# Performance work log

Hardware: AMD Instinct MI355X
Metric: run time of the kernel (lower is better)

## Reference

```python
import jax, jax.numpy as jnp
import numpy as np

B, L, HID, LOW = 1024, 64, 512, 20
TEMP = 1.0
EPS = 1e-20


def setup_inputs() -> dict:
    key = jax.random.key(0)
    ks = jax.random.split(key, 8)
    input_h = jax.random.normal(ks[0], (B, L, HID), jnp.float32)
    input_c = jax.random.normal(ks[1], (B, L, HID), jnp.float32)
    length = jax.random.randint(ks[2], (B,), L // 2, L + 1)          # valid lengths in [L/2, L]
    u_noise = jax.random.uniform(ks[3], (L - 1, B, L - 1), jnp.float32)  # gumbel uniforms per level
    s = 1.0 / np.sqrt(HID)
    W_reduce = jax.random.uniform(ks[4], (HID, LOW), jnp.float32, -s, s)
    b_reduce = jnp.zeros((LOW,), jnp.float32)
    s2 = 1.0 / np.sqrt(2 * LOW)
    W_comp = jax.random.uniform(ks[5], (2 * LOW, 5 * LOW), jnp.float32, -s2, s2)
    b_comp = jnp.zeros((5 * LOW,), jnp.float32)
    query = jax.random.normal(ks[6], (LOW,), jnp.float32) / np.sqrt(LOW)
    return dict(input_h=input_h, input_c=input_c, W_reduce=W_reduce, b_reduce=b_reduce,
                W_comp=W_comp, b_comp=b_comp, query=query, u_noise=u_noise, length=length)


def _treelstm(hl, cl, hr, cr, W, b):
    # BinaryTreeLSTMLayer.forward: concat children, one Linear to 5 gates
    v = jnp.concatenate([hl, hr], axis=-1) @ W + b          # (B, n, 5*LOW)
    i_, fl, fr, u_, o = jnp.split(v, 5, axis=-1)
    c = cl * jax.nn.sigmoid(fl + 1.0) + cr * jax.nn.sigmoid(fr + 1.0) \
        + jnp.tanh(u_) * jax.nn.sigmoid(i_)
    h = jax.nn.sigmoid(o) * jnp.tanh(c)
    return h, c


def _masked_softmax(logits, mask):
    probs = jax.nn.softmax(logits, axis=1)
    probs = probs * mask + EPS
    return probs / probs.sum(axis=1, keepdims=True)


def _st_gumbel(logits, u, mask):
    g = -jnp.log(-jnp.log(u + EPS) + EPS)                   # gumbel noise (non-diff, matches .data)
    y = _masked_softmax((logits + g) / TEMP, mask)
    y_hard = jax.nn.one_hot(jnp.argmax(y, axis=1), y.shape[1], dtype=y.dtype)
    return jax.lax.stop_gradient(y_hard - y) + y            # straight-through


def _forward(input_h, input_c, W_reduce, b_reduce, W_comp, b_comp, query, u_noise, length):
    h = input_h @ W_reduce + b_reduce                       # (B, L, LOW)  reduce_dim
    c = input_c @ W_reduce + b_reduce
    length_mask = (jnp.arange(L)[None, :] < length[:, None]).astype(h.dtype)  # (B, L)
    for i in range(L - 1):                                  # sequential DP over pyramid levels
        hl, cl = h[:, :-1], c[:, :-1]
        hr, cr = h[:, 1:], c[:, 1:]
        nh, nc = _treelstm(hl, cl, hr, cr, W_comp, b_comp)  # (B, L-1-i, LOW) all adjacent merges
        if i < L - 2:
            logits = nh @ query                             # dot_nd scoring, (B, L-1-i)
            sel = _st_gumbel(logits, u_noise[i, :, :L - 1 - i], length_mask[:, i + 1:])
            cum = jnp.cumsum(sel, axis=1)
            left = (1.0 - cum)[..., None]                   # keep old left spans
            right = (cum - sel)[..., None]                  # shift old right spans
            se = sel[..., None]
            nh = se * nh + left * hl + right * hr
            nc = se * nc + left * cl + right * cr
        done = length_mask[:, i + 1][:, None, None]         # update_state done_mask
        h = done * nh + (1.0 - done) * hl
        c = done * nc + (1.0 - done) * cl
    return h[:, 0]                                          # (B, LOW) root hidden state


def reference(input_h, input_c, W_reduce, b_reduce, W_comp, b_comp, query, u_noise, length):
    return _forward(input_h, input_c, W_reduce, b_reduce, W_comp, b_comp, query, u_noise, length)
```

## Files before the change

kernel.cpp:

```cpp
#include <hip/hip_runtime.h>
#include <cmath>
#include <cfloat>

namespace {

constexpr int kB   = 1024;
constexpr int kL   = 64;
constexpr int kHid = 512;
constexpr int kLow = 20;
constexpr int kLM1 = 63;
constexpr int kRowElems = kL * kLow;

typedef float v2f __attribute__((ext_vector_type(2)));

__device__ __forceinline__ float fsig(float x) {
  return __builtin_amdgcn_rcpf(1.0f + __expf(-x));
}
__device__ __forceinline__ float ftanhf(float x) {
  return 1.0f - 2.0f * __builtin_amdgcn_rcpf(1.0f + __expf(2.0f * x));
}
__device__ __forceinline__ int rdl_i(int v, int l) {
  return __builtin_amdgcn_readlane(v, l);
}
__device__ __forceinline__ float rdl_f(float v, int l) {
  return __int_as_float(__builtin_amdgcn_readlane(__float_as_int(v), l));
}

#define DPPI(v, ctrl) __builtin_amdgcn_update_dpp((v), (v), (ctrl), 0xF, 0xF, false)
#define DPPF(v, ctrl) __int_as_float(DPPI(__float_as_int(v), (ctrl)))
#define DPPF0(v, ctrl)                                                        \
  __int_as_float(__builtin_amdgcn_update_dpp(0, __float_as_int(v), (ctrl),    \
                                             0xF, 0xF, true))
#define UMAX_STAGE(CTRL)                                                      \
  {                                                                           \
    const unsigned o_ = (unsigned)DPPI((int)m, CTRL);                         \
    m = (m > o_) ? m : o_;                                                    \
  }

#define PKFMA(ACC, X, W)                                                      \
  asm("v_pk_fma_f32 %0, %1, %2, %0" : "+v"(ACC) : "v"(X), "v"(W))

#define LOGIT_REDUCE(PR_)                                                     \
  {                                                                           \
    PR_ += DPPF0(PR_, 0xB1);                                                  \
    PR_ += DPPF0(PR_, 0x4E);                                                  \
    PR_ += DPPF0(PR_, 0x141);                                                 \
    PR_ += DPPF0(PR_, 0x140);                                                 \
    PR_ += DPPF0(PR_, 0x142);                                                 \
  }

__global__ __launch_bounds__(256, 6)
void reduce_kernel(const float* __restrict__ Xh, const float* __restrict__ Xc,
                   const float* __restrict__ W, const float* __restrict__ bv,
                   float* __restrict__ H0, float* __restrict__ C0) {
  __shared__ float xs[5184];
  __shared__ float wsm[64 * 20];

  const int bid = blockIdx.x;
  const float* __restrict__ X = (bid < kB) ? Xh : Xc;
  float* __restrict__ O       = (bid < kB) ? H0 : C0;
  const int b = bid & (kB - 1);
  X += (size_t)b * kL * kHid;
  O += (size_t)b * kRowElems;

  const int tid  = threadIdx.x;
  const int wave = tid >> 6;
  const int lane = tid & 63;

  float acc[20];
#pragma unroll
  for (int d = 0; d < 20; ++d) acc[d] = 0.0f;

  for (int ch = 0; ch < 8; ++ch) {
    __syncthreads();
#pragma unroll
    for (int r = 0; r < 4; ++r) {
      int f   = r * 256 + tid;
      int row = f >> 4;
      int c4  = (f & 15) << 2;
      float4 v = *(const float4*)(X + row * kHid + ch * 64 + c4);
      *(float4*)(xs + row * 65 + c4) = v;
    }
#pragma unroll
    for (int r = 0; r < 5; ++r) {
      int f = r * 256 + tid;
      wsm[f] = W[ch * 1280 + f];
    }
    __syncthreads();
#pragma unroll
    for (int kk = 0; kk < 16; ++kk) {
      int k = wave * 16 + kk;
      float x = xs[lane * 65 + k];
      const float4* wp = (const float4*)(wsm + k * 20);
      float4 w0 = wp[0], w1 = wp[1], w2 = wp[2], w3 = wp[3], w4 = wp[4];
      acc[0]  = fmaf(x, w0.x, acc[0]);  acc[1]  = fmaf(x, w0.y, acc[1]);
      acc[2]  = fmaf(x, w0.z, acc[2]);  acc[3]  = fmaf(x, w0.w, acc[3]);
      acc[4]  = fmaf(x, w1.x, acc[4]);  acc[5]  = fmaf(x, w1.y, acc[5]);
      acc[6]  = fmaf(x, w1.z, acc[6]);  acc[7]  = fmaf(x, w1.w, acc[7]);
      acc[8]  = fmaf(x, w2.x, acc[8]);  acc[9]  = fmaf(x, w2.y, acc[9]);
      acc[10] = fmaf(x, w2.z, acc[10]); acc[11] = fmaf(x, w2.w, acc[11]);
      acc[12] = fmaf(x, w3.x, acc[12]); acc[13] = fmaf(x, w3.y, acc[13]);
      acc[14] = fmaf(x, w3.z, acc[14]); acc[15] = fmaf(x, w3.w, acc[15]);
      acc[16] = fmaf(x, w4.x, acc[16]); acc[17] = fmaf(x, w4.y, acc[17]);
      acc[18] = fmaf(x, w4.z, acc[18]); acc[19] = fmaf(x, w4.w, acc[19]);
    }
  }

  __syncthreads();
  float* red = xs;
#pragma unroll
  for (int d = 0; d < 20; ++d) red[wave * 1280 + lane * 20 + d] = acc[d];
  __syncthreads();
#pragma unroll
  for (int r = 0; r < 5; ++r) {
    int f = r * 256 + tid;
    float s = (red[f] + red[1280 + f]) + (red[2560 + f] + red[3840 + f]);
    O[f] = s + bv[f % 20];
  }
}

#define EVAL_UNIT(A_, B2_, PS_, DD_, HN_)                                     \
  {                                                                           \
    float ai = bcs[DD_], af = bcs[20 + DD_], ag = bcs[40 + DD_],              \
          au = bcs[60 + DD_], ao = bcs[80 + DD_];                             \
    const int xa_ = (A_)*20, xb_ = (B2_)*20, wr_ = (DD_)*44;                  \
    _Pragma("unroll")                                                         \
    for (int kq = 0; kq < 10; ++kq) {                                         \
      const float4 xq = (kq < 5)                                              \
          ? *(const float4*)(h_state + xa_ + kq * 4)                          \
          : *(const float4*)(h_state + xb_ + (kq - 5) * 4);                   \
      const float4 wi = *(const float4*)(Wt + wr_ + kq * 4);                  \
      const float4 wf = *(const float4*)(Wt + 880  + wr_ + kq * 4);           \
      const float4 wg = *(const float4*)(Wt + 1760 + wr_ + kq * 4);           \
      const float4 wu = *(const float4*)(Wt + 2640 + wr_ + kq * 4);           \
      const float4 wo = *(const float4*)(Wt + 3520 + wr_ + kq * 4);           \
      ai = fmaf(xq.x, wi.x, ai); ai = fmaf(xq.y, wi.y, ai);                   \
      ai = fmaf(xq.z, wi.z, ai); ai = fmaf(xq.w, wi.w, ai);                   \
      af = fmaf(xq.x, wf.x, af); af = fmaf(xq.y, wf.y, af);                   \
      af = fmaf(xq.z, wf.z, af); af = fmaf(xq.w, wf.w, af);                   \
      ag = fmaf(xq.x, wg.x, ag); ag = fmaf(xq.y, wg.y, ag);                   \
      ag = fmaf(xq.z, wg.z, ag); ag = fmaf(xq.w, wg.w, ag);                   \
      au = fmaf(xq.x, wu.x, au); au = fmaf(xq.y, wu.y, au);                   \
      au = fmaf(xq.z, wu.z, au); au = fmaf(xq.w, wu.w, au);                   \
      ao = fmaf(xq.x, wo.x, ao); ao = fmaf(xq.y, wo.y, ao);                   \
      ao = fmaf(xq.z, wo.z, ao); ao = fmaf(xq.w, wo.w, ao);                   \
    }                                                                         \
    const float cl_ = c_state[(A_)*20 + (DD_)],                               \
                cr_ = c_state[(B2_)*20 + (DD_)];                              \
    const float cn_ = cl_ * fsig(af + 1.0f) + cr_ * fsig(ag + 1.0f) +         \
                      ftanhf(au) * fsig(ai);                                  \
    (HN_) = fsig(ao) * ftanhf(cn_);                                           \
    nh[(PS_)*20 + (DD_)] = (HN_);                                             \
    nc[(PS_)*20 + (DD_)] = cn_;                                               \
  }

__global__ __launch_bounds__(64, 1)
void pyramid_kernel(const float* __restrict__ H0, const float* __restrict__ C0,
                    const float* __restrict__ Wc, const float* __restrict__ bcg,
                    const float* __restrict__ query, const float* __restrict__ U,
                    const int* __restrict__ length, float* __restrict__ out) {
  __shared__ float h_state[64 * 20];
  __shared__ float c_state[64 * 20];
  __shared__ float nh[63 * 20];
  __shared__ float nc[63 * 20];
  __shared__ float Wt[100 * 44];
  __shared__ float bcs[100];
  __shared__ float qvs[20];
  __shared__ float sc[200];

  const int b    = blockIdx.x;
  const int lane = threadIdx.x;
  const int p    = lane >> 5;
  const int dd   = lane & 31;
  const int ddc  = dd < 20 ? dd : 19;
  int len = length[b];
  len = len < 1 ? 1 : (len > 64 ? 64 : len);

  {
    const float4* h4 = (const float4*)(H0 + (size_t)b * kRowElems);
    const float4* c4 = (const float4*)(C0 + (size_t)b * kRowElems);
#pragma unroll
    for (int r = 0; r < 5; ++r) {
      int f = r * 64 + lane;
      ((float4*)h_state)[f] = h4[f];
      ((float4*)c_state)[f] = c4[f];
    }
  }
  for (int f = lane; f < 4000; f += 64) {
    int c = f / 40, k = f - c * 40;
    Wt[c * 44 + k] = Wc[k * 100 + c];
  }
  for (int f = lane; f < 100; f += 64) bcs[f] = bcg[f];
  if (lane < 20) qvs[lane] = query[lane];

  const bool cact = lane < 50;
  const int  c0   = cact ? 2 * lane : 0;
  const int  c1   = c0 + 1;
  v2f Wv0[20], Wv1[20];
#pragma unroll
  for (int k2 = 0; k2 < 20; ++k2) {
    Wv0[k2] = (v2f){Wc[(2 * k2) * 100 + c0], Wc[(2 * k2 + 1) * 100 + c0]};
    Wv1[k2] = (v2f){Wc[(2 * k2) * 100 + c1], Wc[(2 * k2 + 1) * 100 + c1]};
  }
  const float bb0 = bcg[c0], bb1 = bcg[c1];
  const float qv_r = query[ddc];

  int   idx_r  = lane;
  int   pidx_r = lane;
  float lgt_r  = -FLT_MAX;

  const int col = lane < 62 ? lane : 62;
  const float u_row0 = U[b * kLM1 + col];
  float u_c = (kLM1 > 1) ? U[1 * (kB * kLM1) + b * kLM1 + col] : 0.0f;

#pragma unroll 1
  for (int r = 0; r < 20; ++r) {
    int uu = r * 64 + lane;
    if (uu < 1260) {
      int pp = uu / 20, d2 = uu - pp * 20;
      float hn_;
      EVAL_UNIT(pp, pp + 1, pp, d2, hn_);
      (void)hn_;
    }
  }
  if (lane < 63) {
    float s = 0.0f;
#pragma unroll
    for (int q = 0; q < 5; ++q) {
      const float4 t  = *(const float4*)(nh  + lane * 20 + q * 4);
      const float4 qv = *(const float4*)(qvs + q * 4);
      s = fmaf(t.x, qv.x, s); s = fmaf(t.y, qv.y, s);
      s = fmaf(t.z, qv.z, s); s = fmaf(t.w, qv.w, s);
    }
    lgt_r = s;
  }

  float gcur = -__logf(-__logf(u_row0 + 1e-20f) + 1e-20f);

  const int nIter = len - 1;
#pragma unroll 1
  for (int i = 0; i < nIter; ++i) {
    const int n = kL - i;

    const float zf = lgt_r + gcur;
    const unsigned ub = __float_as_uint(zf);
    unsigned key = ((int)ub < 0) ? ~ub : (ub | 0x80000000u);
    const bool valid = (lane <= n - 2) && ((i + 1 + lane) < len);
    if (!valid) key = 0u;
    unsigned m = key;
    UMAX_STAGE(0xB1);
    UMAX_STAGE(0x4E);
    UMAX_STAGE(0x141);
    UMAX_STAGE(0x140);
    UMAX_STAGE(0x142);
    UMAX_STAGE(0x143);
    const unsigned gmax = (unsigned)rdl_i((int)m, 63);
    const unsigned long long bal = __ballot(valid && (key == gmax));
    const int k = (int)(__ffsll(bal) - 1);

    float u_d = 0.0f;
    if (i + 2 <= kLM1 - 1) u_d = U[(i + 2) * (kB * kLM1) + b * kLM1 + col];

    const int km1 = (k >= 1) ? k - 1 : 0;
    const int kp2 = (k <= n - 3) ? k + 2 : 0;
    const int tgt = rdl_i(idx_r,  k);
    const int psk = rdl_i(pidx_r, k);
    const int iA  = rdl_i(idx_r,  km1);
    const int pA  = rdl_i(pidx_r, km1);
    const int iB  = rdl_i(idx_r,  kp2);

    if (lane < 20) {
      h_state[tgt * 20 + lane] = nh[psk * 20 + lane];
      c_state[tgt * 20 + lane] = nc[psk * 20 + lane];
    }

    {
      int   sI = DPPI(idx_r,  0x101);
      int   sP = DPPI(pidx_r, 0x101);
      float sL = DPPF(lgt_r,  0x101);
      const int   bi16 = rdl_i(idx_r, 16),  bi32 = rdl_i(idx_r, 32),
                  bi48 = rdl_i(idx_r, 48);
      const int   bp16 = rdl_i(pidx_r, 16), bp32 = rdl_i(pidx_r, 32),
                  bp48 = rdl_i(pidx_r, 48);
      const float bl16 = rdl_f(lgt_r, 16),  bl32 = rdl_f(lgt_r, 32),
                  bl48 = rdl_f(lgt_r, 48);
      if (lane == 15) { sI = bi16; sP = bp16; sL = bl16; }
      if (lane == 31) { sI = bi32; sP = bp32; sL = bl32; }
      if (lane == 47) { sI = bi48; sP = bp48; sL = bl48; }
      const bool doI = (lane >= k + 1) && (lane <= n - 2);
      const bool doP = (lane >= k + 1) && (lane <= n - 3);
      if (doI) idx_r = sI;
      if (doP) { pidx_r = sP; lgt_r = sL; }
    }

    if (i < len - 2) {
      const bool hasA = (k >= 1);
      const bool hasB = (k <= n - 3);

      v2f hA2[10], hT2[10], hB2[10];
#pragma unroll
      for (int q = 0; q < 5; ++q) {
        const float4 tA = *(const float4*)(h_state + iA * 20 + q * 4);
        const float4 tT = *(const float4*)(nh + psk * 20 + q * 4);
        const float4 tB = *(const float4*)(h_state + iB * 20 + q * 4);
        hA2[2*q]   = (v2f){tA.x, tA.y};  hA2[2*q+1] = (v2f){tA.z, tA.w};
        hT2[2*q]   = (v2f){tT.x, tT.y};  hT2[2*q+1] = (v2f){tT.z, tT.w};
        hB2[2*q]   = (v2f){tB.x, tB.y};  hB2[2*q+1] = (v2f){tB.z, tB.w};
      }

      v2f aA0 = (v2f){0.f, 0.f}, aA1 = aA0, aB0 = aA0, aB1 = aA0;
#pragma unroll
      for (int k2 = 0; k2 < 10; ++k2) {
        PKFMA(aA0, hA2[k2], Wv0[k2]);
        PKFMA(aA1, hA2[k2], Wv1[k2]);
        PKFMA(aB0, hT2[k2], Wv0[k2]);
        PKFMA(aB1, hT2[k2], Wv1[k2]);
      }
#pragma unroll
      for (int k2 = 10; k2 < 20; ++k2) {
        PKFMA(aA0, hT2[k2 - 10], Wv0[k2]);
        PKFMA(aA1, hT2[k2 - 10], Wv1[k2]);
        PKFMA(aB0, hB2[k2 - 10], Wv0[k2]);
        PKFMA(aB1, hB2[k2 - 10], Wv1[k2]);
      }

      if (cact) {
        *(v2f*)(sc + c0)       = (v2f){aA0[0] + aA0[1] + bb0,
                                       aA1[0] + aA1[1] + bb1};
        *(v2f*)(sc + 100 + c0) = (v2f){aB0[0] + aB0[1] + bb0,
                                       aB1[0] + aB1[1] + bb1};
      }

      const float* scp = sc + p * 100;
      const float i_ = scp[ddc],      fl_ = scp[20 + ddc],
                  fr_ = scp[40 + ddc], u_ = scp[60 + ddc],
                  o_ = scp[80 + ddc];
      const float cl_ = (p == 0) ? c_state[iA * 20 + ddc] : nc[psk * 20 + ddc];
      const float cr_ = (p == 0) ? nc[psk * 20 + ddc] : c_state[iB * 20 + ddc];
      const float cn_ = cl_ * fsig(fl_ + 1.0f) + cr_ * fsig(fr_ + 1.0f) +
                        ftanhf(u_) * fsig(i_);
      const float hn_ = fsig(o_) * ftanhf(cn_);
      const int   slot = (p == 0) ? pA : psk;
      const bool  mine = (p == 0) ? hasA : hasB;
      if (mine && dd < 20) {
        nh[slot * 20 + dd] = hn_;
        nc[slot * 20 + dd] = cn_;
      }
      float pr = (dd < 20) ? hn_ * qv_r : 0.0f;
      LOGIT_REDUCE(pr);
      const float vA = rdl_f(pr, 31);
      const float vB = rdl_f(pr, 63);
      if (hasA && lane == k - 1) lgt_r = vA;
      if (hasB && lane == k)     lgt_r = vB;
    }

    gcur = -__logf(-__logf(u_c + 1e-20f) + 1e-20f);
    u_c  = u_d;
  }

  const int root = rdl_i(idx_r, 0);
  if (lane < 20) {
    out[b * 20 + lane] = h_state[root * 20 + lane];
  }
}

}

extern "C" void kernel_launch(void* const* d_in, const int* in_sizes, int n_in,
                              void* d_out, int out_size, void* d_ws, size_t ws_size,
                              hipStream_t stream) {
  const float* input_h  = (const float*)d_in[0];
  const float* input_c  = (const float*)d_in[1];
  const float* W_reduce = (const float*)d_in[2];
  const float* b_reduce = (const float*)d_in[3];
  const float* W_comp   = (const float*)d_in[4];
  const float* b_comp   = (const float*)d_in[5];
  const float* query    = (const float*)d_in[6];
  const float* u_noise  = (const float*)d_in[7];
  const int*   length   = (const int*)d_in[8];
  float* out = (float*)d_out;

  float* H0 = (float*)d_ws;
  float* C0 = H0 + (size_t)kB * kL * kLow;

  reduce_kernel<<<dim3(2 * kB), dim3(256), 0, stream>>>(
      input_h, input_c, W_reduce, b_reduce, H0, C0);
  pyramid_kernel<<<dim3(kB), dim3(64), 0, stream>>>(
      H0, C0, W_comp, b_comp, query, u_noise, length, out);
}
```

Baseline: 159.1 us.

## Read reduce weights via scalar loads and hoist child state loads above writes

In the reduce kernel, the weight tile is no longer staged in shared memory. Each wave now reads its weight row directly from global memory at a wave-uniform address, which lets the compiler use scalar loads, and the inner k loop is kept rolled. In the tree kernel, the loads of the left, target and right child h/c vectors are moved before the state writeback so their LDS latency overlaps the selection bookkeeping. The risk is that the uniform global loads add latency or that the extra live registers lower occupancy. Hoisting the loads above the writes also relies on them reading values that the writeback does not change.

```diff
diff --git a/kernel.cpp b/kernel.cpp
--- a/kernel.cpp
+++ b/kernel.cpp
@@ -54,7 +54,6 @@
                    const float* __restrict__ W, const float* __restrict__ bv,
                    float* __restrict__ H0, float* __restrict__ C0) {
   __shared__ float xs[5184];
-  __shared__ float wsm[64 * 20];
 
   const int bid = blockIdx.x;
   const float* __restrict__ X = (bid < kB) ? Xh : Xc;
@@ -64,7 +63,7 @@
   O += (size_t)b * kRowElems;
 
   const int tid  = threadIdx.x;
-  const int wave = tid >> 6;
+  const int wave = __builtin_amdgcn_readfirstlane(tid >> 6);
   const int lane = tid & 63;
 
   float acc[20];
@@ -81,28 +80,14 @@
       float4 v = *(const float4*)(X + row * kHid + ch * 64 + c4);
       *(float4*)(xs + row * 65 + c4) = v;
     }
-#pragma unroll
-    for (int r = 0; r < 5; ++r) {
-      int f = r * 256 + tid;
-      wsm[f] = W[ch * 1280 + f];
-    }
     __syncthreads();
-#pragma unroll
+#pragma unroll 1
     for (int kk = 0; kk < 16; ++kk) {
-      int k = wave * 16 + kk;
-      float x = xs[lane * 65 + k];
-      const float4* wp = (const float4*)(wsm + k * 20);
-      float4 w0 = wp[0], w1 = wp[1], w2 = wp[2], w3 = wp[3], w4 = wp[4];
-      acc[0]  = fmaf(x, w0.x, acc[0]);  acc[1]  = fmaf(x, w0.y, acc[1]);
-      acc[2]  = fmaf(x, w0.z, acc[2]);  acc[3]  = fmaf(x, w0.w, acc[3]);
-      acc[4]  = fmaf(x, w1.x, acc[4]);  acc[5]  = fmaf(x, w1.y, acc[5]);
-      acc[6]  = fmaf(x, w1.z, acc[6]);  acc[7]  = fmaf(x, w1.w, acc[7]);
-      acc[8]  = fmaf(x, w2.x, acc[8]);  acc[9]  = fmaf(x, w2.y, acc[9]);
-      acc[10] = fmaf(x, w2.z, acc[10]); acc[11] = fmaf(x, w2.w, acc[11]);
-      acc[12] = fmaf(x, w3.x, acc[12]); acc[13] = fmaf(x, w3.y, acc[13]);
-      acc[14] = fmaf(x, w3.z, acc[14]); acc[15] = fmaf(x, w3.w, acc[15]);
-      acc[16] = fmaf(x, w4.x, acc[16]); acc[17] = fmaf(x, w4.y, acc[17]);
-      acc[18] = fmaf(x, w4.z, acc[18]); acc[19] = fmaf(x, w4.w, acc[19]);
+      const int k = wave * 16 + kk;
+      const float x = xs[lane * 65 + k];
+      const float* __restrict__ wr = W + ch * 1280 + k * 20;
+#pragma unroll
+      for (int d = 0; d < 20; ++d) acc[d] = fmaf(x, wr[d], acc[d]);
     }
   }
 
@@ -269,6 +254,20 @@
     const int pA  = rdl_i(pidx_r, km1);
     const int iB  = rdl_i(idx_r,  kp2);
 
+    v2f hA2[10], hT2[10], hB2[10];
+#pragma unroll
+    for (int q = 0; q < 5; ++q) {
+      const float4 tA = *(const float4*)(h_state + iA * 20 + q * 4);
+      const float4 tT = *(const float4*)(nh + psk * 20 + q * 4);
+      const float4 tB = *(const float4*)(h_state + iB * 20 + q * 4);
+      hA2[2*q]   = (v2f){tA.x, tA.y};  hA2[2*q+1] = (v2f){tA.z, tA.w};
+      hT2[2*q]   = (v2f){tT.x, tT.y};  hT2[2*q+1] = (v2f){tT.z, tT.w};
+      hB2[2*q]   = (v2f){tB.x, tB.y};  hB2[2*q+1] = (v2f){tB.z, tB.w};
+    }
+    const float cA_ = c_state[iA * 20 + ddc];
+    const float cT_ = nc[psk * 20 + ddc];
+    const float cB_ = c_state[iB * 20 + ddc];
+
     if (lane < 20) {
       h_state[tgt * 20 + lane] = nh[psk * 20 + lane];
       c_state[tgt * 20 + lane] = nc[psk * 20 + lane];
@@ -297,17 +296,6 @@
       const bool hasA = (k >= 1);
       const bool hasB = (k <= n - 3);
 
-      v2f hA2[10], hT2[10], hB2[10];
-#pragma unroll
-      for (int q = 0; q < 5; ++q) {
-        const float4 tA = *(const float4*)(h_state + iA * 20 + q * 4);
-        const float4 tT = *(const float4*)(nh + psk * 20 + q * 4);
-        const float4 tB = *(const float4*)(h_state + iB * 20 + q * 4);
-        hA2[2*q]   = (v2f){tA.x, tA.y};  hA2[2*q+1] = (v2f){tA.z, tA.w};
-        hT2[2*q]   = (v2f){tT.x, tT.y};  hT2[2*q+1] = (v2f){tT.z, tT.w};
-        hB2[2*q]   = (v2f){tB.x, tB.y};  hB2[2*q+1] = (v2f){tB.z, tB.w};
-      }
-
       v2f aA0 = (v2f){0.f, 0.f}, aA1 = aA0, aB0 = aA0, aB1 = aA0;
 #pragma unroll
       for (int k2 = 0; k2 < 10; ++k2) {
@@ -335,8 +323,8 @@
       const float i_ = scp[ddc],      fl_ = scp[20 + ddc],
                   fr_ = scp[40 + ddc], u_ = scp[60 + ddc],
                   o_ = scp[80 + ddc];
-      const float cl_ = (p == 0) ? c_state[iA * 20 + ddc] : nc[psk * 20 + ddc];
-      const float cr_ = (p == 0) ? nc[psk * 20 + ddc] : c_state[iB * 20 + ddc];
+      const float cl_ = (p == 0) ? cA_ : cT_;
+      const float cr_ = (p == 0) ? cT_ : cB_;
       const float cn_ = cl_ * fsig(fl_ + 1.0f) + cr_ * fsig(fr_ + 1.0f) +
                         ftanhf(u_) * fsig(i_);
       const float hn_ = fsig(o_) * ftanhf(cn_);
```

After: 188.2 us. 1.18x slower.

## Process two batch rows per wavefront to interleave independent serial chains

Applied to the files above, without the earlier changes.

Each 64-lane block now handles two batch rows, A and B, and interleaves their serial pyramid iterations (argmax, merge, shift, packed FMA, nonlinearity) so the latency of one row's dependent steps can be hidden by the other row's instructions. The grid is halved to 512 blocks. In exchange, LDS use per block roughly doubles, register pressure rises, and a pair of rows runs for the longer of their two lengths, with the shorter row masked by active flags. The intent is to raise instruction-level parallelism in this latency-bound sequential loop.

```diff
diff --git a/kernel.cpp b/kernel.cpp
--- a/kernel.cpp
+++ b/kernel.cpp
@@ -119,39 +119,162 @@
   }
 }
 
-#define EVAL_UNIT(A_, B2_, PS_, DD_, HN_)                                     \
-  {                                                                           \
-    float ai = bcs[DD_], af = bcs[20 + DD_], ag = bcs[40 + DD_],              \
-          au = bcs[60 + DD_], ao = bcs[80 + DD_];                             \
-    const int xa_ = (A_)*20, xb_ = (B2_)*20, wr_ = (DD_)*44;                  \
+#define EVAL_UNIT2(PP_, DD_)                                                  \
+  {                                                                           \
+    float aiA = bcs[DD_], afA = bcs[20 + DD_], agA = bcs[40 + DD_],           \
+          auA = bcs[60 + DD_], aoA = bcs[80 + DD_];                           \
+    float aiB = aiA, afB = afA, agB = agA, auB = auA, aoB = aoA;              \
+    const int xa_ = (PP_)*20, xb_ = (PP_ + 1)*20, wr_ = (DD_)*44;             \
     _Pragma("unroll")                                                         \
     for (int kq = 0; kq < 10; ++kq) {                                         \
-      const float4 xq = (kq < 5)                                              \
-          ? *(const float4*)(h_state + xa_ + kq * 4)                          \
-          : *(const float4*)(h_state + xb_ + (kq - 5) * 4);                   \
+      const float4 xqA = (kq < 5)                                             \
+          ? *(const float4*)(h_sA + xa_ + kq * 4)                             \
+          : *(const float4*)(h_sA + xb_ + (kq - 5) * 4);                      \
+      const float4 xqB = (kq < 5)                                             \
+          ? *(const float4*)(h_sB + xa_ + kq * 4)                             \
+          : *(const float4*)(h_sB + xb_ + (kq - 5) * 4);                      \
       const float4 wi = *(const float4*)(Wt + wr_ + kq * 4);                  \
       const float4 wf = *(const float4*)(Wt + 880  + wr_ + kq * 4);           \
       const float4 wg = *(const float4*)(Wt + 1760 + wr_ + kq * 4);           \
       const float4 wu = *(const float4*)(Wt + 2640 + wr_ + kq * 4);           \
       const float4 wo = *(const float4*)(Wt + 3520 + wr_ + kq * 4);           \
-      ai = fmaf(xq.x, wi.x, ai); ai = fmaf(xq.y, wi.y, ai);                   \
-      ai = fmaf(xq.z, wi.z, ai); ai = fmaf(xq.w, wi.w, ai);                   \
-      af = fmaf(xq.x, wf.x, af); af = fmaf(xq.y, wf.y, af);                   \
-      af = fmaf(xq.z, wf.z, af); af = fmaf(xq.w, wf.w, af);                   \
-      ag = fmaf(xq.x, wg.x, ag); ag = fmaf(xq.y, wg.y, ag);                   \
-      ag = fmaf(xq.z, wg.z, ag); ag = fmaf(xq.w, wg.w, ag);                   \
-      au = fmaf(xq.x, wu.x, au); au = fmaf(xq.y, wu.y, au);                   \
-      au = fmaf(xq.z, wu.z, au); au = fmaf(xq.w, wu.w, au);                   \
-      ao = fmaf(xq.x, wo.x, ao); ao = fmaf(xq.y, wo.y, ao);                   \
-      ao = fmaf(xq.z, wo.z, ao); ao = fmaf(xq.w, wo.w, ao);                   \
-    }                                                                         \
-    const float cl_ = c_state[(A_)*20 + (DD_)],                               \
-                cr_ = c_state[(B2_)*20 + (DD_)];                              \
-    const float cn_ = cl_ * fsig(af + 1.0f) + cr_ * fsig(ag + 1.0f) +         \
-                      ftanhf(au) * fsig(ai);                                  \
-    (HN_) = fsig(ao) * ftanhf(cn_);                                           \
-    nh[(PS_)*20 + (DD_)] = (HN_);                                             \
-    nc[(PS_)*20 + (DD_)] = cn_;                                               \
+      aiA = fmaf(xqA.x, wi.x, aiA); aiA = fmaf(xqA.y, wi.y, aiA);             \
+      aiA = fmaf(xqA.z, wi.z, aiA); aiA = fmaf(xqA.w, wi.w, aiA);             \
+      afA = fmaf(xqA.x, wf.x, afA); afA = fmaf(xqA.y, wf.y, afA);             \
+      afA = fmaf(xqA.z, wf.z, afA); afA = fmaf(xqA.w, wf.w, afA);             \
+      agA = fmaf(xqA.x, wg.x, agA); agA = fmaf(xqA.y, wg.y, agA);             \
+      agA = fmaf(xqA.z, wg.z, agA); agA = fmaf(xqA.w, wg.w, agA);             \
+      auA = fmaf(xqA.x, wu.x, auA); auA = fmaf(xqA.y, wu.y, auA);             \
+      auA = fmaf(xqA.z, wu.z, auA); auA = fmaf(xqA.w, wu.w, auA);             \
+      aoA = fmaf(xqA.x, wo.x, aoA); aoA = fmaf(xqA.y, wo.y, aoA);             \
+      aoA = fmaf(xqA.z, wo.z, aoA); aoA = fmaf(xqA.w, wo.w, aoA);             \
+      aiB = fmaf(xqB.x, wi.x, aiB); aiB = fmaf(xqB.y, wi.y, aiB);             \
+      aiB = fmaf(xqB.z, wi.z, aiB); aiB = fmaf(xqB.w, wi.w, aiB);             \
+      afB = fmaf(xqB.x, wf.x, afB); afB = fmaf(xqB.y, wf.y, afB);             \
+      afB = fmaf(xqB.z, wf.z, afB); afB = fmaf(xqB.w, wf.w, afB);             \
+      agB = fmaf(xqB.x, wg.x, agB); agB = fmaf(xqB.y, wg.y, agB);             \
+      agB = fmaf(xqB.z, wg.z, agB); agB = fmaf(xqB.w, wg.w, agB);             \
+      auB = fmaf(xqB.x, wu.x, auB); auB = fmaf(xqB.y, wu.y, auB);             \
+      auB = fmaf(xqB.z, wu.z, auB); auB = fmaf(xqB.w, wu.w, auB);             \
+      aoB = fmaf(xqB.x, wo.x, aoB); aoB = fmaf(xqB.y, wo.y, aoB);             \
+      aoB = fmaf(xqB.z, wo.z, aoB); aoB = fmaf(xqB.w, wo.w, aoB);             \
+    }                                                                         \
+    {                                                                         \
+      const float clA = c_sA[(PP_)*20 + (DD_)],                               \
+                  crA = c_sA[(PP_+1)*20 + (DD_)];                             \
+      const float cnA = clA * fsig(afA + 1.0f) + crA * fsig(agA + 1.0f) +     \
+                        ftanhf(auA) * fsig(aiA);                              \
+      const float hnA = fsig(aoA) * ftanhf(cnA);                              \
+      nhA[(PP_)*20 + (DD_)] = hnA;  ncA[(PP_)*20 + (DD_)] = cnA;              \
+      const float clB = c_sB[(PP_)*20 + (DD_)],                               \
+                  crB = c_sB[(PP_+1)*20 + (DD_)];                             \
+      const float cnB = clB * fsig(afB + 1.0f) + crB * fsig(agB + 1.0f) +     \
+                        ftanhf(auB) * fsig(aiB);                              \
+      const float hnB = fsig(aoB) * ftanhf(cnB);                              \
+      nhB[(PP_)*20 + (DD_)] = hnB;  ncB[(PP_)*20 + (DD_)] = cnB;              \
+    }                                                                         \
+  }
+
+#define ROW_ARGMAX(LGT_, G_, LEN_, KOUT_)                                     \
+  {                                                                           \
+    const float zf = (LGT_) + (G_);                                           \
+    const unsigned ub = __float_as_uint(zf);                                  \
+    unsigned key = ((int)ub < 0) ? ~ub : (ub | 0x80000000u);                  \
+    const bool valid = (lane <= n - 2) && ((i + 1 + lane) < (LEN_));          \
+    if (!valid) key = 0u;                                                     \
+    unsigned m = key;                                                         \
+    UMAX_STAGE(0xB1); UMAX_STAGE(0x4E); UMAX_STAGE(0x141);                    \
+    UMAX_STAGE(0x140); UMAX_STAGE(0x142); UMAX_STAGE(0x143);                  \
+    const unsigned gmax = (unsigned)rdl_i((int)m, 63);                        \
+    const unsigned long long bal = __ballot(valid && (key == gmax));          \
+    (KOUT_) = bal ? (int)(__ffsll(bal) - 1) : 0;                              \
+  }
+
+#define ROW_HOIST(HS, CS, NH, NC, IL_, IR_, PSK_, XL, XT, XR, CL_, CT_, CR_)  \
+  {                                                                           \
+    _Pragma("unroll")                                                         \
+    for (int q = 0; q < 5; ++q) {                                             \
+      const float4 tL = *(const float4*)((HS) + (IL_)*20 + q * 4);            \
+      const float4 tT = *(const float4*)((NH) + (PSK_)*20 + q * 4);           \
+      const float4 tR = *(const float4*)((HS) + (IR_)*20 + q * 4);            \
+      XL[2*q] = (v2f){tL.x, tL.y}; XL[2*q+1] = (v2f){tL.z, tL.w};             \
+      XT[2*q] = (v2f){tT.x, tT.y}; XT[2*q+1] = (v2f){tT.z, tT.w};             \
+      XR[2*q] = (v2f){tR.x, tR.y}; XR[2*q+1] = (v2f){tR.z, tR.w};             \
+    }                                                                         \
+    CL_ = (CS)[(IL_)*20 + ddc];                                               \
+    CT_ = (NC)[(PSK_)*20 + ddc];                                              \
+    CR_ = (CS)[(IR_)*20 + ddc];                                               \
+  }
+
+#define ROW_MERGE(HS, CS, NH, NC, TGT_, PSK_, ACT_)                           \
+  if ((ACT_) && lane < 20) {                                                  \
+    (HS)[(TGT_)*20 + lane] = (NH)[(PSK_)*20 + lane];                          \
+    (CS)[(TGT_)*20 + lane] = (NC)[(PSK_)*20 + lane];                          \
+  }
+
+#define ROW_SHIFT(IDX_, PIDX_, LGT_, K_, ACT_)                                \
+  {                                                                           \
+    int   sI = DPPI(IDX_,  0x101);                                            \
+    int   sP = DPPI(PIDX_, 0x101);                                            \
+    float sL = DPPF(LGT_,  0x101);                                            \
+    const int   b16i = rdl_i(IDX_, 16),  b32i = rdl_i(IDX_, 32),              \
+                b48i = rdl_i(IDX_, 48);                                       \
+    const int   b16p = rdl_i(PIDX_, 16), b32p = rdl_i(PIDX_, 32),             \
+                b48p = rdl_i(PIDX_, 48);                                      \
+    const float b16l = rdl_f(LGT_, 16),  b32l = rdl_f(LGT_, 32),              \
+                b48l = rdl_f(LGT_, 48);                                       \
+    if (lane == 15) { sI = b16i; sP = b16p; sL = b16l; }                      \
+    if (lane == 31) { sI = b32i; sP = b32p; sL = b32l; }                      \
+    if (lane == 47) { sI = b48i; sP = b48p; sL = b48l; }                      \
+    const bool doI = (ACT_) && (lane >= (K_) + 1) && (lane <= n - 2);         \
+    const bool doP = (ACT_) && (lane >= (K_) + 1) && (lane <= n - 3);         \
+    if (doI) IDX_ = sI;                                                       \
+    if (doP) { PIDX_ = sP; LGT_ = sL; }                                       \
+  }
+
+#define ROW_FMASC(XL, XT, XR, SC)                                             \
+  {                                                                           \
+    v2f a0 = (v2f){0.f, 0.f}, a1 = a0, b0 = a0, b1 = a0;                      \
+    _Pragma("unroll")                                                         \
+    for (int k2 = 0; k2 < 10; ++k2) {                                         \
+      PKFMA(a0, XL[k2], Wv0[k2]);                                             \
+      PKFMA(a1, XL[k2], Wv1[k2]);                                             \
+      PKFMA(b0, XT[k2], Wv0[k2]);                                             \
+      PKFMA(b1, XT[k2], Wv1[k2]);                                             \
+    }                                                                         \
+    _Pragma("unroll")                                                         \
+    for (int k2 = 10; k2 < 20; ++k2) {                                        \
+      PKFMA(a0, XT[k2 - 10], Wv0[k2]);                                        \
+      PKFMA(a1, XT[k2 - 10], Wv1[k2]);                                        \
+      PKFMA(b0, XR[k2 - 10], Wv0[k2]);                                        \
+      PKFMA(b1, XR[k2 - 10], Wv1[k2]);                                        \
+    }                                                                         \
+    if (cact) {                                                               \
+      *(v2f*)((SC) + c0)       = (v2f){a0[0]+a0[1]+bb0, a1[0]+a1[1]+bb1};     \
+      *(v2f*)((SC) + 100 + c0) = (v2f){b0[0]+b0[1]+bb0, b1[0]+b1[1]+bb1};     \
+    }                                                                         \
+  }
+
+#define ROW_NONLIN(SC, CL_, CT_, CR_, NH, NC, PL_, PSK_, K_, EV_, LGT_)       \
+  {                                                                           \
+    const bool hasL = (K_) >= 1, hasR = (K_) <= n - 3;                        \
+    const float* scp = (SC) + p * 100;                                        \
+    const float gi = scp[ddc], gfl = scp[20 + ddc], gfr = scp[40 + ddc],      \
+                gu = scp[60 + ddc], go = scp[80 + ddc];                       \
+    const float cl_ = (p == 0) ? (CL_) : (CT_);                               \
+    const float cr_ = (p == 0) ? (CT_) : (CR_);                               \
+    const float cn_ = cl_ * fsig(gfl + 1.0f) + cr_ * fsig(gfr + 1.0f) +       \
+                      ftanhf(gu) * fsig(gi);                                  \
+    const float hn_ = fsig(go) * ftanhf(cn_);                                 \
+    const int   slot = (p == 0) ? (PL_) : (PSK_);                             \
+    const bool  mine = (EV_) && ((p == 0) ? hasL : hasR);                     \
+    if (mine && dd < 20) { (NH)[slot*20 + dd] = hn_; (NC)[slot*20 + dd] = cn_; } \
+    float pr = (dd < 20) ? hn_ * qv_r : 0.0f;                                 \
+    LOGIT_REDUCE(pr);                                                         \
+    const float vL = rdl_f(pr, 31);                                           \
+    const float vR = rdl_f(pr, 63);                                           \
+    if ((EV_) && hasL && lane == (K_) - 1) (LGT_) = vL;                       \
+    if ((EV_) && hasR && lane == (K_))     (LGT_) = vR;                       \
   }
 
 __global__ __launch_bounds__(64, 1)
@@ -159,31 +282,36 @@
                     const float* __restrict__ Wc, const float* __restrict__ bcg,
                     const float* __restrict__ query, const float* __restrict__ U,
                     const int* __restrict__ length, float* __restrict__ out) {
-  __shared__ float h_state[64 * 20];
-  __shared__ float c_state[64 * 20];
-  __shared__ float nh[63 * 20];
-  __shared__ float nc[63 * 20];
+  __shared__ float h_sA[64 * 20], c_sA[64 * 20], nhA[63 * 20], ncA[63 * 20];
+  __shared__ float h_sB[64 * 20], c_sB[64 * 20], nhB[63 * 20], ncB[63 * 20];
   __shared__ float Wt[100 * 44];
   __shared__ float bcs[100];
   __shared__ float qvs[20];
-  __shared__ float sc[200];
-
-  const int b    = blockIdx.x;
+  __shared__ float scA[200], scB[200];
+
+  const int bblk = blockIdx.x;
+  const int rowA = 2 * bblk, rowB = 2 * bblk + 1;
   const int lane = threadIdx.x;
   const int p    = lane >> 5;
   const int dd   = lane & 31;
   const int ddc  = dd < 20 ? dd : 19;
-  int len = length[b];
-  len = len < 1 ? 1 : (len > 64 ? 64 : len);
+  int lenA = length[rowA];
+  lenA = lenA < 1 ? 1 : (lenA > 64 ? 64 : lenA);
+  int lenB = length[rowB];
+  lenB = lenB < 1 ? 1 : (lenB > 64 ? 64 : lenB);
 
   {
-    const float4* h4 = (const float4*)(H0 + (size_t)b * kRowElems);
-    const float4* c4 = (const float4*)(C0 + (size_t)b * kRowElems);
+    const float4* h4A = (const float4*)(H0 + (size_t)rowA * kRowElems);
+    const float4* c4A = (const float4*)(C0 + (size_t)rowA * kRowElems);
+    const float4* h4B = (const float4*)(H0 + (size_t)rowB * kRowElems);
+    const float4* c4B = (const float4*)(C0 + (size_t)rowB * kRowElems);
 #pragma unroll
     for (int r = 0; r < 5; ++r) {
       int f = r * 64 + lane;
-      ((float4*)h_state)[f] = h4[f];
-      ((float4*)c_state)[f] = c4[f];
+      ((float4*)h_sA)[f] = h4A[f];
+      ((float4*)c_sA)[f] = c4A[f];
+      ((float4*)h_sB)[f] = h4B[f];
+      ((float4*)c_sB)[f] = c4B[f];
     }
   }
   for (int f = lane; f < 4000; f += 64) {
@@ -205,162 +333,103 @@
   const float bb0 = bcg[c0], bb1 = bcg[c1];
   const float qv_r = query[ddc];
 
-  int   idx_r  = lane;
-  int   pidx_r = lane;
-  float lgt_r  = -FLT_MAX;
+  int   idxA = lane, pidxA = lane;
+  int   idxB = lane, pidxB = lane;
+  float lgtA = -FLT_MAX, lgtB = -FLT_MAX;
 
   const int col = lane < 62 ? lane : 62;
-  const float u_row0 = U[b * kLM1 + col];
-  float u_c = (kLM1 > 1) ? U[1 * (kB * kLM1) + b * kLM1 + col] : 0.0f;
+  const float u0A = U[rowA * kLM1 + col];
+  const float u0B = U[rowB * kLM1 + col];
+  float u_cA = U[(size_t)1 * (kB * kLM1) + rowA * kLM1 + col];
+  float u_cB = U[(size_t)1 * (kB * kLM1) + rowB * kLM1 + col];
 
 #pragma unroll 1
   for (int r = 0; r < 20; ++r) {
     int uu = r * 64 + lane;
     if (uu < 1260) {
       int pp = uu / 20, d2 = uu - pp * 20;
-      float hn_;
-      EVAL_UNIT(pp, pp + 1, pp, d2, hn_);
-      (void)hn_;
+      EVAL_UNIT2(pp, d2);
     }
   }
   if (lane < 63) {
-    float s = 0.0f;
+    float sA = 0.0f, sB = 0.0f;
 #pragma unroll
     for (int q = 0; q < 5; ++q) {
-      const float4 t  = *(const float4*)(nh  + lane * 20 + q * 4);
       const float4 qv = *(const float4*)(qvs + q * 4);
-      s = fmaf(t.x, qv.x, s); s = fmaf(t.y, qv.y, s);
-      s = fmaf(t.z, qv.z, s); s = fmaf(t.w, qv.w, s);
-    }
-    lgt_r = s;
-  }
-
-  float gcur = -__logf(-__logf(u_row0 + 1e-20f) + 1e-20f);
-
-  const int nIter = len - 1;
+      const float4 tA = *(const float4*)(nhA + lane * 20 + q * 4);
+      const float4 tB = *(const float4*)(nhB + lane * 20 + q * 4);
+      sA = fmaf(tA.x, qv.x, sA); sA = fmaf(tA.y, qv.y, sA);
+      sA = fmaf(tA.z, qv.z, sA); sA = fmaf(tA.w, qv.w, sA);
+      sB = fmaf(tB.x, qv.x, sB); sB = fmaf(tB.y, qv.y, sB);
+      sB = fmaf(tB.z, qv.z, sB); sB = fmaf(tB.w, qv.w, sB);
+    }
+    lgtA = sA;
+    lgtB = sB;
+  }
+
+  float gA = -__logf(-__logf(u0A + 1e-20f) + 1e-20f);
+  float gB = -__logf(-__logf(u0B + 1e-20f) + 1e-20f);
+
+  const int maxIter = (lenA > lenB ? lenA : lenB) - 1;
 #pragma unroll 1
-  for (int i = 0; i < nIter; ++i) {
+  for (int i = 0; i < maxIter; ++i) {
     const int n = kL - i;
-
-    const float zf = lgt_r + gcur;
-    const unsigned ub = __float_as_uint(zf);
-    unsigned key = ((int)ub < 0) ? ~ub : (ub | 0x80000000u);
-    const bool valid = (lane <= n - 2) && ((i + 1 + lane) < len);
-    if (!valid) key = 0u;
-    unsigned m = key;
-    UMAX_STAGE(0xB1);
-    UMAX_STAGE(0x4E);
-    UMAX_STAGE(0x141);
-    UMAX_STAGE(0x140);
-    UMAX_STAGE(0x142);
-    UMAX_STAGE(0x143);
-    const unsigned gmax = (unsigned)rdl_i((int)m, 63);
-    const unsigned long long bal = __ballot(valid && (key == gmax));
-    const int k = (int)(__ffsll(bal) - 1);
-
-    float u_d = 0.0f;
-    if (i + 2 <= kLM1 - 1) u_d = U[(i + 2) * (kB * kLM1) + b * kLM1 + col];
-
-    const int km1 = (k >= 1) ? k - 1 : 0;
-    const int kp2 = (k <= n - 3) ? k + 2 : 0;
-    const int tgt = rdl_i(idx_r,  k);
-    const int psk = rdl_i(pidx_r, k);
-    const int iA  = rdl_i(idx_r,  km1);
-    const int pA  = rdl_i(pidx_r, km1);
-    const int iB  = rdl_i(idx_r,  kp2);
-
-    if (lane < 20) {
-      h_state[tgt * 20 + lane] = nh[psk * 20 + lane];
-      c_state[tgt * 20 + lane] = nc[psk * 20 + lane];
-    }
+    const bool actA = i < lenA - 1, actB = i < lenB - 1;
+    const bool evA  = i < lenA - 2, evB  = i < lenB - 2;
+
+    int kA, kB2;
+    ROW_ARGMAX(lgtA, gA, lenA, kA);
+    ROW_ARGMAX(lgtB, gB, lenB, kB2);
+
+    float u_dA = 0.0f, u_dB = 0.0f;
+    if (i + 2 < kLM1) {
+      u_dA = U[(size_t)(i + 2) * (kB * kLM1) + rowA * kLM1 + col];
+      u_dB = U[(size_t)(i + 2) * (kB * kLM1) + rowB * kLM1 + col];
+    }
+
+    const int A_km1 = kA >= 1 ? kA - 1 : 0;
+    const int A_kp2 = kA <= n - 3 ? kA + 2 : 0;
+    const int A_tgt = rdl_i(idxA, kA),   A_psk = rdl_i(pidxA, kA);
+    const int A_iL  = rdl_i(idxA, A_km1), A_pL = rdl_i(pidxA, A_km1);
+    const int A_iR  = rdl_i(idxA, A_kp2);
+    const int B_km1 = kB2 >= 1 ? kB2 - 1 : 0;
+    const int B_kp2 = kB2 <= n - 3 ? kB2 + 2 : 0;
+    const int B_tgt = rdl_i(idxB, kB2),   B_psk = rdl_i(pidxB, kB2);
+    const int B_iL  = rdl_i(idxB, B_km1), B_pL = rdl_i(pidxB, B_km1);
+    const int B_iR  = rdl_i(idxB, B_kp2);
 
     {
-      int   sI = DPPI(idx_r,  0x101);
-      int   sP = DPPI(pidx_r, 0x101);
-      float sL = DPPF(lgt_r,  0x101);
-      const int   bi16 = rdl_i(idx_r, 16),  bi32 = rdl_i(idx_r, 32),
-                  bi48 = rdl_i(idx_r, 48);
-      const int   bp16 = rdl_i(pidx_r, 16), bp32 = rdl_i(pidx_r, 32),
-                  bp48 = rdl_i(pidx_r, 48);
-      const float bl16 = rdl_f(lgt_r, 16),  bl32 = rdl_f(lgt_r, 32),
-                  bl48 = rdl_f(lgt_r, 48);
-      if (lane == 15) { sI = bi16; sP = bp16; sL = bl16; }
-      if (lane == 31) { sI = bi32; sP = bp32; sL = bl32; }
-      if (lane == 47) { sI = bi48; sP = bp48; sL = bl48; }
-      const bool doI = (lane >= k + 1) && (lane <= n - 2);
-      const bool doP = (lane >= k + 1) && (lane <= n - 3);
-      if (doI) idx_r = sI;
-      if (doP) { pidx_r = sP; lgt_r = sL; }
-    }
-
-    if (i < len - 2) {
-      const bool hasA = (k >= 1);
-      const bool hasB = (k <= n - 3);
-
-      v2f hA2[10], hT2[10], hB2[10];
-#pragma unroll
-      for (int q = 0; q < 5; ++q) {
-        const float4 tA = *(const float4*)(h_state + iA * 20 + q * 4);
-        const float4 tT = *(const float4*)(nh + psk * 20 + q * 4);
-        const float4 tB = *(const float4*)(h_state + iB * 20 + q * 4);
-        hA2[2*q]   = (v2f){tA.x, tA.y};  hA2[2*q+1] = (v2f){tA.z, tA.w};
-        hT2[2*q]   = (v2f){tT.x, tT.y};  hT2[2*q+1] = (v2f){tT.z, tT.w};
-        hB2[2*q]   = (v2f){tB.x, tB.y};  hB2[2*q+1] = (v2f){tB.z, tB.w};
-      }
-
-      v2f aA0 = (v2f){0.f, 0.f}, aA1 = aA0, aB0 = aA0, aB1 = aA0;
-#pragma unroll
-      for (int k2 = 0; k2 < 10; ++k2) {
-        PKFMA(aA0, hA2[k2], Wv0[k2]);
-        PKFMA(aA1, hA2[k2], Wv1[k2]);
-        PKFMA(aB0, hT2[k2], Wv0[k2]);
-        PKFMA(aB1, hT2[k2], Wv1[k2]);
-      }
-#pragma unroll
-      for (int k2 = 10; k2 < 20; ++k2) {
-        PKFMA(aA0, hT2[k2 - 10], Wv0[k2]);
-        PKFMA(aA1, hT2[k2 - 10], Wv1[k2]);
-        PKFMA(aB0, hB2[k2 - 10], Wv0[k2]);
-        PKFMA(aB1, hB2[k2 - 10], Wv1[k2]);
-      }
-
-      if (cact) {
-        *(v2f*)(sc + c0)       = (v2f){aA0[0] + aA0[1] + bb0,
-                                       aA1[0] + aA1[1] + bb1};
-        *(v2f*)(sc + 100 + c0) = (v2f){aB0[0] + aB0[1] + bb0,
-                                       aB1[0] + aB1[1] + bb1};
-      }
-
-      const float* scp = sc + p * 100;
-      const float i_ = scp[ddc],      fl_ = scp[20 + ddc],
-                  fr_ = scp[40 + ddc], u_ = scp[60 + ddc],
-                  o_ = scp[80 + ddc];
-      const float cl_ = (p == 0) ? c_state[iA * 20 + ddc] : nc[psk * 20 + ddc];
-      const float cr_ = (p == 0) ? nc[psk * 20 + ddc] : c_state[iB * 20 + ddc];
-      const float cn_ = cl_ * fsig(fl_ + 1.0f) + cr_ * fsig(fr_ + 1.0f) +
-                        ftanhf(u_) * fsig(i_);
-      const float hn_ = fsig(o_) * ftanhf(cn_);
-      const int   slot = (p == 0) ? pA : psk;
-      const bool  mine = (p == 0) ? hasA : hasB;
-      if (mine && dd < 20) {
-        nh[slot * 20 + dd] = hn_;
-        nc[slot * 20 + dd] = cn_;
-      }
-      float pr = (dd < 20) ? hn_ * qv_r : 0.0f;
-      LOGIT_REDUCE(pr);
-      const float vA = rdl_f(pr, 31);
-      const float vB = rdl_f(pr, 63);
-      if (hasA && lane == k - 1) lgt_r = vA;
-      if (hasB && lane == k)     lgt_r = vB;
-    }
-
-    gcur = -__logf(-__logf(u_c + 1e-20f) + 1e-20f);
-    u_c  = u_d;
-  }
-
-  const int root = rdl_i(idx_r, 0);
+      v2f A_xL[10], A_xT[10], A_xR[10];
+      float A_cL, A_cT, A_cR;
+      ROW_HOIST(h_sA, c_sA, nhA, ncA, A_iL, A_iR, A_psk,
+                A_xL, A_xT, A_xR, A_cL, A_cT, A_cR);
+      ROW_MERGE(h_sA, c_sA, nhA, ncA, A_tgt, A_psk, actA);
+      ROW_SHIFT(idxA, pidxA, lgtA, kA, actA);
+      ROW_FMASC(A_xL, A_xT, A_xR, scA);
+
+      v2f B_xL[10], B_xT[10], B_xR[10];
+      float B_cL, B_cT, B_cR;
+      ROW_HOIST(h_sB, c_sB, nhB, ncB, B_iL, B_iR, B_psk,
+                B_xL, B_xT, B_xR, B_cL, B_cT, B_cR);
+      ROW_MERGE(h_sB, c_sB, nhB, ncB, B_tgt, B_psk, actB);
+      ROW_SHIFT(idxB, pidxB, lgtB, kB2, actB);
+      ROW_FMASC(B_xL, B_xT, B_xR, scB);
+
+      ROW_NONLIN(scA, A_cL, A_cT, A_cR, nhA, ncA, A_pL, A_psk, kA, evA, lgtA);
+      ROW_NONLIN(scB, B_cL, B_cT, B_cR, nhB, ncB, B_pL, B_psk, kB2, evB, lgtB);
+    }
+
+    gA = -__logf(-__logf(u_cA + 1e-20f) + 1e-20f);
+    gB = -__logf(-__logf(u_cB + 1e-20f) + 1e-20f);
+    u_cA = u_dA;
+    u_cB = u_dB;
+  }
+
+  const int rootA = rdl_i(idxA, 0);
+  const int rootB = rdl_i(idxB, 0);
   if (lane < 20) {
-    out[b * 20 + lane] = h_state[root * 20 + lane];
+    out[rowA * 20 + lane] = h_sA[rootA * 20 + lane];
+    out[rowB * 20 + lane] = h_sB[rootB * 20 + lane];
   }
 }
 
@@ -385,6 +454,6 @@
 
   reduce_kernel<<<dim3(2 * kB), dim3(256), 0, stream>>>(
       input_h, input_c, W_reduce, b_reduce, H0, C0);
-  pyramid_kernel<<<dim3(kB), dim3(64), 0, stream>>>(
+  pyramid_kernel<<<dim3(kB / 2), dim3(64), 0, stream>>>(
       H0, C0, W_comp, b_comp, query, u_noise, length, out);
 }
```

Result: slower. 216.1 us (+35.8%).
